# Kernel optimization log

Hardware: AMD Instinct MI355X
Metric: run time of the kernel (lower is better)

Reference implementation:

```python
import jax, jax.numpy as jnp
import numpy as np

T = 50000
SPIN_LEN = 365
TRAIN_LEN = 40000
ML = 2.9086   # PET normalization mean
SL = 1.898    # PET normalization std


def setup_inputs() -> dict:
    key = jax.random.key(0)
    ks = jax.random.split(key, 8)
    return {
        "x": jax.random.uniform(ks[0], (T, 1, 2), dtype=jnp.float32),
        "y_obs": jax.random.uniform(ks[1], (T, 1), dtype=jnp.float32),
        "weight_r_yom": jax.random.uniform(ks[2], (1, 1), dtype=jnp.float32),
        "weight_r_ylm": jax.random.uniform(ks[3], (1, 1), dtype=jnp.float32),
        "weight_r_yfm": jax.random.uniform(ks[4], (1, 1), dtype=jnp.float32),
        "bias_b0_ylm": jax.random.uniform(ks[5], (1,), dtype=jnp.float32),
        "weight_b2_ylm": jax.random.uniform(ks[6], (1, 1), dtype=jnp.float32),
        "theltaC": jax.random.uniform(ks[7], (1, 1), dtype=jnp.float32),
        "epoch": 1,
        "time_lag": 1,
    }


def _run(x, y_obs, wom, wlm, wfm, b0, b2, thC, time_lag):
    # x: [T, 1, 2] (time, seq_len=1, features); loop index 'b' in torch code is time.
    u1 = x[:, 0, 0]  # [T] mass input (precip)
    u2 = x[:, 0, 1]  # [T] PET forcing
    n = u1.shape[0]

    eo = jnp.exp(wom[0, 0])
    el = jnp.exp(wlm[0, 0])
    ef = jnp.exp(wfm[0, 0])
    den = eo + el + ef
    oo = eo / den      # output gate (constant over time)
    ol1 = el / den     # loss-gate scale (constant)
    b0s = b0[0]
    b2s = b2[0, 0]
    _ = thC  # theltaC only feeds px->ib, and ib is overwritten with 0 in the source

    def step(c0, inp):
        idx, u1t, u2t = inp
        ol3 = b0s + (u2t - ML) / SL * b2s
        ol = ol1 * jax.nn.sigmoid(ol3)
        c_safe = jnp.where(c0 > 0, c0, 1.0)
        olc_pre = jnp.where(c0 > 0, ol - jax.nn.elu(ol - u2t / c_safe), ol)
        f = jax.nn.relu(1.0 - oo - olc_pre)   # f uses pre-relu ol_constraint
        olc = jax.nn.relu(olc_pre)
        c1 = f * c0 + u1t                      # ib == 0 => (1-ib)*g == g
        active = idx >= time_lag
        c1 = jnp.where(active, c1, c0)
        zero = 0.0 * c0
        # h_n(=h0+bp0=h0), c_n, l_n, lc_n, bp_n, Gate_ib, Gate_oo, Gate_ol, Gate_olc, Gate_f
        outs = jnp.stack([oo * c0, c0, ol * c0, olc * c0, zero, zero,
                          oo + zero, ol, olc, f])
        return c1, outs

    idxs = jnp.arange(n)
    _, outs = jax.lax.scan(step, jnp.float32(0.0), (idxs, u1, u2))  # outs: [T,10]
    mask = (idxs >= time_lag)[:, None]
    outs = jnp.where(mask, outs, 0.0)

    h_n, c_n, l_n, lc_n, bp_n, g_ib, g_oo, g_ol, g_olc, g_f = [
        outs[:, i:i + 1] for i in range(10)
    ]

    # torch.std is unbiased (ddof=1)
    obsstd = jnp.std(y_obs[SPIN_LEN:TRAIN_LEN], ddof=1)
    obs_std = jnp.where(mask, obsstd, 0.0)
    h_nout = jnp.concatenate([h_n, obs_std], axis=1)

    return (h_n, c_n, l_n, lc_n, bp_n, g_ib, g_oo, g_ol, g_olc, g_f,
            h_nout, obs_std)


def reference(x, y_obs, weight_r_yom, weight_r_ylm, weight_r_yfm,
              bias_b0_ylm, weight_b2_ylm, theltaC, epoch, time_lag):
    return _run(x, y_obs, weight_r_yom, weight_r_ylm, weight_r_yfm,
                bias_b0_ylm, weight_b2_ylm, theltaC, time_lag)
```

## Files before the change

### kernel.cpp

```cpp
#include <hip/hip_runtime.h>
#include <hip/hip_bf16.h>

#define SPIN_LEN 365
#define TRAIN_LEN 40000
#define ML 2.9086f
#define SL 1.898f
#define L2E 1.4426950408889634f

#define WARM 64
#define BLK 256
#define NENT (BLK + WARM)

#define STD_N     (TRAIN_LEN - SPIN_LEN)
#define STD_BODY4 ((TRAIN_LEN - 368) >> 2)
#define STD_FULL  38
#define STD_TAIL  (STD_BODY4 - STD_FULL * BLK)

#define EXP2F(v) __builtin_amdgcn_exp2f(v)

__global__ __launch_bounds__(BLK) void fused_kernel(
        const float* __restrict__ x, const float* __restrict__ y,
        const float* __restrict__ wom, const float* __restrict__ wlm,
        const float* __restrict__ wfm, const float* __restrict__ b0,
        const float* __restrict__ b2, const int* __restrict__ tlp,
        float* __restrict__ out, int T) {
    const int tid = threadIdx.x;
    const int t0  = blockIdx.x * BLK;
    const int t   = t0 + tid;
    int tl = tlp[0]; if (tl < 0) tl = 0;

    float eo = __expf(wom[0]);
    float el = __expf(wlm[0]);
    float ef = __expf(wfm[0]);
    float iden = __builtin_amdgcn_rcpf(eo + el + ef);
    float oo   = eo * iden;
    float ol1  = el * iden;
    float koo  = 1.0f - oo;
    float sb2  = b2[0] * (1.0f / SL);
    float base = fmaf(-ML, sb2, b0[0]);

    __shared__ float4 ent[NENT];
    __shared__ float sh1[BLK / 64], sh2[BLK / 64];

    const float2* xp = (const float2*)x;
    int ia = t0 - WARM + tid;
    ia = ia < 0 ? 0 : (ia > T - 1 ? T - 1 : ia);
    float2 ua = xp[ia];
    float2 ub;
    if (tid < NENT - BLK) {
        int ib = t0 - WARM + BLK + tid;
        ib = ib > T - 1 ? T - 1 : ib;
        ub = xp[ib];
    }

    const float4* y4 = (const float4*)(y + 368);
    float s1 = 0.0f, s2 = 0.0f;
    #pragma unroll
    for (int k = 0; k < STD_FULL; ++k) {
        float4 v = y4[tid + (k << 8)];
        float a0 = v.x - 0.5f, a1 = v.y - 0.5f, a2 = v.z - 0.5f, a3 = v.w - 0.5f;
        s1 += (a0 + a1) + (a2 + a3);
        s2 = fmaf(a0, a0, fmaf(a1, a1, fmaf(a2, a2, fmaf(a3, a3, s2))));
    }
    if (tid < STD_TAIL) {
        float4 v = y4[tid + STD_FULL * BLK];
        float a0 = v.x - 0.5f, a1 = v.y - 0.5f, a2 = v.z - 0.5f, a3 = v.w - 0.5f;
        s1 += (a0 + a1) + (a2 + a3);
        s2 = fmaf(a0, a0, fmaf(a1, a1, fmaf(a2, a2, fmaf(a3, a3, s2))));
    }
    if (tid < 3) {
        float v = y[SPIN_LEN + tid] - 0.5f;
        s1 += v; s2 = fmaf(v, v, s2);
    }

    {
        float ol3 = fmaf(ua.y, sb2, base);
        float sig = __builtin_amdgcn_rcpf(1.0f + EXP2F(-ol3 * L2E));
        float ol  = ol1 * sig;
        ent[tid] = make_float4(ua.x, ua.y, ol, koo - ol - 1.0f);
        if (tid < NENT - BLK) {
            float ol3b = fmaf(ub.y, sb2, base);
            float sigb = __builtin_amdgcn_rcpf(1.0f + EXP2F(-ol3b * L2E));
            float olb  = ol1 * sigb;
            ent[BLK + tid] = make_float4(ub.x, ub.y, olb, koo - olb - 1.0f);
        }
    }

    for (int o = 32; o > 0; o >>= 1) {
        s1 += __shfl_down(s1, o, 64);
        s2 += __shfl_down(s2, o, 64);
    }
    int wave = tid >> 6;
    if ((tid & 63) == 0) { sh1[wave] = s1; sh2[wave] = s2; }

    __syncthreads();

    float S1 = (sh1[0] + sh1[1]) + (sh1[2] + sh1[3]);
    float S2 = (sh2[0] + sh2[1]) + (sh2[2] + sh2[3]);
    float nf = (float)STD_N;
    float obsstd = sqrtf(fmaxf((S2 - S1 * S1 / nf) / (nf - 1.0f), 0.0f));

    float c = 0.0f;
    float4 e = ent[tid];
    #pragma unroll 8
    for (int k = 0; k < WARM; ++k) {
        float4 en = ent[tid + k + 1];
        float u1 = e.x, u2 = e.y, ol = e.z, qq = e.w;
        bool  cpos = c > 0.0f;
        float E    = EXP2F(fmaf(-u2 * L2E, __builtin_amdgcn_rcpf(cpos ? c : 1.0f), ol * L2E));
        float c1B  = fmaf(fmaxf(qq + E, 0.0f), c, u1);
        float c1A  = fmaxf(fmaf(koo, c, -u2), 0.0f) + u1;
        float c1   = cpos ? ((ol * c > u2) ? c1A : c1B) : u1;
        int i = t - WARM + k;
        c = (i >= tl) ? c1 : c;
        e = en;
    }

    if (t >= T) return;

    float u2 = e.y, ol = e.z;
    bool  cpos = c > 0.0f;
    float rc   = __builtin_amdgcn_rcpf(cpos ? c : 1.0f);
    float E    = EXP2F(fmaf(-u2 * L2E, rc, ol * L2E));
    float olc_pre = cpos ? ((ol * c > u2) ? u2 * rc : (ol + 1.0f - E)) : ol;
    float f   = fmaxf(koo - olc_pre, 0.0f);
    float olc = fmaxf(olc_pre, 0.0f);

    bool mask = t >= tl;
    float h  = mask ? oo * c : 0.0f;
    float sv = mask ? obsstd : 0.0f;

    size_t Ts = (size_t)T;
    out[t]            = h;
    out[Ts + t]       = mask ? c : 0.0f;
    out[2 * Ts + t]   = mask ? ol * c : 0.0f;
    out[3 * Ts + t]   = mask ? olc * c : 0.0f;
    out[4 * Ts + t]   = 0.0f;
    out[5 * Ts + t]   = 0.0f;
    out[6 * Ts + t]   = mask ? oo : 0.0f;
    out[7 * Ts + t]   = mask ? ol : 0.0f;
    out[8 * Ts + t]   = mask ? olc : 0.0f;
    out[9 * Ts + t]   = mask ? f : 0.0f;
    ((float2*)(out + 10 * Ts))[t] = make_float2(h, sv);
    out[12 * Ts + t]  = sv;
}

extern "C" void kernel_launch(void* const* d_in, const int* in_sizes, int n_in,
                              void* d_out, int out_size, void* d_ws, size_t ws_size,
                              hipStream_t stream) {
    const float* x   = (const float*)d_in[0];
    const float* y   = (const float*)d_in[1];
    const float* wom = (const float*)d_in[2];
    const float* wlm = (const float*)d_in[3];
    const float* wfm = (const float*)d_in[4];
    const float* b0  = (const float*)d_in[5];
    const float* b2  = (const float*)d_in[6];
    const int* tl = (const int*)d_in[9];
    float* out = (float*)d_out;
    int T = in_sizes[1];

    fused_kernel<<<(T + BLK - 1) / BLK, BLK, 0, stream>>>(
        x, y, wom, wlm, wfm, b0, b2, tl, out, T);
}
```

Measured before the change: 12.64 us.

## Move std reduction to dedicated block and add fast warmup path

The redundant per-block reduction of y_obs std is moved into one extra block, which computes it once and writes the obs_std columns for all timesteps. Interior blocks whose warm-up window lies fully past time_lag and inside T take a fast path that skips the c>0 and index checks, starting c from the first input. ol is also stored pre-scaled by log2(e) so the loop does fewer multiplies. The trade-off is one block doing a long serial strided write, and the fast path assumes c stays positive.

```diff
diff --git a/kernel.cpp b/kernel.cpp
--- a/kernel.cpp
+++ b/kernel.cpp
@@ -6,6 +6,7 @@
 #define ML 2.9086f
 #define SL 1.898f
 #define L2E 1.4426950408889634f
+#define LN2 0.6931471805599453f
 
 #define WARM 64
 #define BLK 256
@@ -17,6 +18,7 @@
 #define STD_TAIL  (STD_BODY4 - STD_FULL * BLK)
 
 #define EXP2F(v) __builtin_amdgcn_exp2f(v)
+#define RCPF(v)  __builtin_amdgcn_rcpf(v)
 
 __global__ __launch_bounds__(BLK) void fused_kernel(
         const float* __restrict__ x, const float* __restrict__ y,
@@ -25,14 +27,62 @@
         const float* __restrict__ b2, const int* __restrict__ tlp,
         float* __restrict__ out, int T) {
     const int tid = threadIdx.x;
-    const int t0  = blockIdx.x * BLK;
-    const int t   = t0 + tid;
+    const int b   = blockIdx.x;
+    const int NB  = (int)gridDim.x - 1;
     int tl = tlp[0]; if (tl < 0) tl = 0;
+    size_t Ts = (size_t)T;
+
+    if (b == NB) {
+        const float4* y4 = (const float4*)(y + 368);
+        float s1a = 0.f, s1b = 0.f, s2a = 0.f, s2b = 0.f, s2c = 0.f, s2d = 0.f;
+        #pragma unroll
+        for (int k = 0; k < STD_FULL; ++k) {
+            float4 v = y4[tid + (k << 8)];
+            float a0 = v.x - 0.5f, a1 = v.y - 0.5f, a2 = v.z - 0.5f, a3 = v.w - 0.5f;
+            s1a += a0 + a1; s1b += a2 + a3;
+            s2a = fmaf(a0, a0, s2a); s2b = fmaf(a1, a1, s2b);
+            s2c = fmaf(a2, a2, s2c); s2d = fmaf(a3, a3, s2d);
+        }
+        if (tid < STD_TAIL) {
+            float4 v = y4[tid + STD_FULL * BLK];
+            float a0 = v.x - 0.5f, a1 = v.y - 0.5f, a2 = v.z - 0.5f, a3 = v.w - 0.5f;
+            s1a += a0 + a1; s1b += a2 + a3;
+            s2a = fmaf(a0, a0, s2a); s2b = fmaf(a1, a1, s2b);
+            s2c = fmaf(a2, a2, s2c); s2d = fmaf(a3, a3, s2d);
+        }
+        if (tid < 3) {
+            float v = y[SPIN_LEN + tid] - 0.5f;
+            s1a += v; s2a = fmaf(v, v, s2a);
+        }
+        float s1 = s1a + s1b;
+        float s2 = (s2a + s2b) + (s2c + s2d);
+        for (int o = 32; o > 0; o >>= 1) {
+            s1 += __shfl_down(s1, o, 64);
+            s2 += __shfl_down(s2, o, 64);
+        }
+        __shared__ float sh1[BLK / 64], sh2[BLK / 64];
+        int wave = tid >> 6;
+        if ((tid & 63) == 0) { sh1[wave] = s1; sh2[wave] = s2; }
+        __syncthreads();
+        float S1 = (sh1[0] + sh1[1]) + (sh1[2] + sh1[3]);
+        float S2 = (sh2[0] + sh2[1]) + (sh2[2] + sh2[3]);
+        float nf = (float)STD_N;
+        float sv = sqrtf(fmaxf((S2 - S1 * S1 / nf) / (nf - 1.0f), 0.0f));
+        for (int i = tid; i < T; i += BLK) {
+            float svi = (i >= tl) ? sv : 0.0f;
+            out[12 * Ts + i] = svi;
+            out[10 * Ts + 2 * (size_t)i + 1] = svi;
+        }
+        return;
+    }
+
+    const int t0 = b * BLK;
+    const int t  = t0 + tid;
 
     float eo = __expf(wom[0]);
     float el = __expf(wlm[0]);
     float ef = __expf(wfm[0]);
-    float iden = __builtin_amdgcn_rcpf(eo + el + ef);
+    float iden = RCPF(eo + el + ef);
     float oo   = eo * iden;
     float ol1  = el * iden;
     float koo  = 1.0f - oo;
@@ -40,97 +90,84 @@
     float base = fmaf(-ML, sb2, b0[0]);
 
     __shared__ float4 ent[NENT];
-    __shared__ float sh1[BLK / 64], sh2[BLK / 64];
-
     const float2* xp = (const float2*)x;
+    const bool fast = (t0 - WARM >= tl) && (t0 + BLK + WARM <= T);
+
     int ia = t0 - WARM + tid;
-    ia = ia < 0 ? 0 : (ia > T - 1 ? T - 1 : ia);
+    int ib = ia + BLK;
+    if (!fast) {
+        ia = ia < 0 ? 0 : (ia > T - 1 ? T - 1 : ia);
+        ib = ib > T - 1 ? T - 1 : ib;
+    }
     float2 ua = xp[ia];
-    float2 ub;
-    if (tid < NENT - BLK) {
-        int ib = t0 - WARM + BLK + tid;
-        ib = ib > T - 1 ? T - 1 : ib;
-        ub = xp[ib];
-    }
-
-    const float4* y4 = (const float4*)(y + 368);
-    float s1 = 0.0f, s2 = 0.0f;
-    #pragma unroll
-    for (int k = 0; k < STD_FULL; ++k) {
-        float4 v = y4[tid + (k << 8)];
-        float a0 = v.x - 0.5f, a1 = v.y - 0.5f, a2 = v.z - 0.5f, a3 = v.w - 0.5f;
-        s1 += (a0 + a1) + (a2 + a3);
-        s2 = fmaf(a0, a0, fmaf(a1, a1, fmaf(a2, a2, fmaf(a3, a3, s2))));
-    }
-    if (tid < STD_TAIL) {
-        float4 v = y4[tid + STD_FULL * BLK];
-        float a0 = v.x - 0.5f, a1 = v.y - 0.5f, a2 = v.z - 0.5f, a3 = v.w - 0.5f;
-        s1 += (a0 + a1) + (a2 + a3);
-        s2 = fmaf(a0, a0, fmaf(a1, a1, fmaf(a2, a2, fmaf(a3, a3, s2))));
-    }
-    if (tid < 3) {
-        float v = y[SPIN_LEN + tid] - 0.5f;
-        s1 += v; s2 = fmaf(v, v, s2);
-    }
+    float2 ub = make_float2(0.f, 0.f);
+    if (tid < WARM) ub = xp[ib];
 
     {
         float ol3 = fmaf(ua.y, sb2, base);
-        float sig = __builtin_amdgcn_rcpf(1.0f + EXP2F(-ol3 * L2E));
+        float sig = RCPF(1.0f + EXP2F(-ol3 * L2E));
         float ol  = ol1 * sig;
-        ent[tid] = make_float4(ua.x, ua.y, ol, koo - ol - 1.0f);
-        if (tid < NENT - BLK) {
+        ent[tid] = make_float4(ua.x, ua.y, ol * L2E, koo - ol - 1.0f);
+        if (tid < WARM) {
             float ol3b = fmaf(ub.y, sb2, base);
-            float sigb = __builtin_amdgcn_rcpf(1.0f + EXP2F(-ol3b * L2E));
+            float sigb = RCPF(1.0f + EXP2F(-ol3b * L2E));
             float olb  = ol1 * sigb;
-            ent[BLK + tid] = make_float4(ub.x, ub.y, olb, koo - olb - 1.0f);
-        }
-    }
-
-    for (int o = 32; o > 0; o >>= 1) {
-        s1 += __shfl_down(s1, o, 64);
-        s2 += __shfl_down(s2, o, 64);
-    }
-    int wave = tid >> 6;
-    if ((tid & 63) == 0) { sh1[wave] = s1; sh2[wave] = s2; }
-
+            ent[BLK + tid] = make_float4(ub.x, ub.y, olb * L2E, koo - olb - 1.0f);
+        }
+    }
     __syncthreads();
 
-    float S1 = (sh1[0] + sh1[1]) + (sh1[2] + sh1[3]);
-    float S2 = (sh2[0] + sh2[1]) + (sh2[2] + sh2[3]);
-    float nf = (float)STD_N;
-    float obsstd = sqrtf(fmaxf((S2 - S1 * S1 / nf) / (nf - 1.0f), 0.0f));
-
-    float c = 0.0f;
-    float4 e = ent[tid];
-    #pragma unroll 8
-    for (int k = 0; k < WARM; ++k) {
-        float4 en = ent[tid + k + 1];
-        float u1 = e.x, u2 = e.y, ol = e.z, qq = e.w;
-        bool  cpos = c > 0.0f;
-        float E    = EXP2F(fmaf(-u2 * L2E, __builtin_amdgcn_rcpf(cpos ? c : 1.0f), ol * L2E));
-        float c1B  = fmaf(fmaxf(qq + E, 0.0f), c, u1);
-        float c1A  = fmaxf(fmaf(koo, c, -u2), 0.0f) + u1;
-        float c1   = cpos ? ((ol * c > u2) ? c1A : c1B) : u1;
-        int i = t - WARM + k;
-        c = (i >= tl) ? c1 : c;
-        e = en;
+    float c;
+    float4 e;
+    if (fast) {
+        c = ent[tid].x;
+        e = ent[tid + 1];
+        #pragma unroll 7
+        for (int k = 1; k < WARM; ++k) {
+            float4 en = ent[tid + k + 1];
+            float u1 = e.x, u2 = e.y, olL = e.z, qq = e.w;
+            float rc  = RCPF(c);
+            float u2L = u2 * L2E;
+            float E   = EXP2F(fmaf(-u2L, rc, olL));
+            float c1B = fmaf(fmaxf(qq + E, 0.0f), c, u1);
+            float c1A = fmaxf(fmaf(koo, c, -u2), 0.0f) + u1;
+            c = (olL * c > u2L) ? c1A : c1B;
+            e = en;
+        }
+    } else {
+        c = 0.0f;
+        e = ent[tid];
+        #pragma unroll 4
+        for (int k = 0; k < WARM; ++k) {
+            float4 en = ent[tid + k + 1];
+            float u1 = e.x, u2 = e.y, olL = e.z, qq = e.w;
+            bool  cpos = c > 0.0f;
+            float rc  = RCPF(cpos ? c : 1.0f);
+            float u2L = u2 * L2E;
+            float E   = EXP2F(fmaf(-u2L, rc, olL));
+            float c1B = fmaf(fmaxf(qq + E, 0.0f), c, u1);
+            float c1A = fmaxf(fmaf(koo, c, -u2), 0.0f) + u1;
+            float c1  = cpos ? ((olL * c > u2L) ? c1A : c1B) : u1;
+            int i = t - WARM + k;
+            c = (i >= tl) ? c1 : c;
+            e = en;
+        }
     }
 
     if (t >= T) return;
 
-    float u2 = e.y, ol = e.z;
+    float u2 = e.y, olL = e.z;
+    float ol = olL * LN2;
     bool  cpos = c > 0.0f;
-    float rc   = __builtin_amdgcn_rcpf(cpos ? c : 1.0f);
-    float E    = EXP2F(fmaf(-u2 * L2E, rc, ol * L2E));
-    float olc_pre = cpos ? ((ol * c > u2) ? u2 * rc : (ol + 1.0f - E)) : ol;
+    float rc   = RCPF(cpos ? c : 1.0f);
+    float E    = EXP2F(fmaf(-u2 * L2E, rc, olL));
+    float olc_pre = cpos ? ((olL * c > u2 * L2E) ? u2 * rc : (ol + 1.0f - E)) : ol;
     float f   = fmaxf(koo - olc_pre, 0.0f);
     float olc = fmaxf(olc_pre, 0.0f);
 
     bool mask = t >= tl;
-    float h  = mask ? oo * c : 0.0f;
-    float sv = mask ? obsstd : 0.0f;
-
-    size_t Ts = (size_t)T;
+    float h = mask ? oo * c : 0.0f;
+
     out[t]            = h;
     out[Ts + t]       = mask ? c : 0.0f;
     out[2 * Ts + t]   = mask ? ol * c : 0.0f;
@@ -141,8 +178,7 @@
     out[7 * Ts + t]   = mask ? ol : 0.0f;
     out[8 * Ts + t]   = mask ? olc : 0.0f;
     out[9 * Ts + t]   = mask ? f : 0.0f;
-    ((float2*)(out + 10 * Ts))[t] = make_float2(h, sv);
-    out[12 * Ts + t]  = sv;
+    out[10 * Ts + 2 * (size_t)t] = h;
 }
 
 extern "C" void kernel_launch(void* const* d_in, const int* in_sizes, int n_in,
@@ -159,6 +195,7 @@
     float* out = (float*)d_out;
     int T = in_sizes[1];
 
-    fused_kernel<<<(T + BLK - 1) / BLK, BLK, 0, stream>>>(
+    int nb = (T + BLK - 1) / BLK;
+    fused_kernel<<<nb + 1, BLK, 0, stream>>>(
         x, y, wom, wlm, wfm, b0, b2, tl, out, T);
 }
```

Result: slower. 16.05 us (+27.0%).
